# Kernel tuning notes

Hardware: AMD Instinct MI355X
Metric: run time of the kernel (lower is better)

Reference implementation:

```python
import jax, jax.numpy as jnp
import numpy as np

# torch.optim.Adam defaults
LR = 1e-3
B1 = 0.9
B2 = 0.999
EPS = 1e-8


def setup_inputs() -> dict:
    key = jax.random.key(0)
    k1, k2 = jax.random.split(key)
    B, N_train, d = 128, 16384, 1024
    h = jax.random.normal(k1, (B, d), dtype=jnp.float32)
    H_train = jax.random.normal(k2, (N_train, d), dtype=jnp.float32)
    return {"h": h, "H_train": H_train, "n_epoch": 1000}


def reference(h, H_train, n_epoch):
    # preweights: [B, N_train], optimized by Adam for n_epoch steps
    B, N_train = h.shape[0], H_train.shape[0]

    def loss_fn(p):
        w = jax.nn.softmax(p, axis=-1)          # [B, N_train]
        H_approx = w @ H_train                   # [B, d]
        return jnp.sum((H_approx - h) ** 2)

    grad_fn = jax.grad(loss_fn)

    def step(carry, t):
        p, m, v = carry
        g = grad_fn(p)
        m = B1 * m + (1.0 - B1) * g
        v = B2 * v + (1.0 - B2) * (g * g)
        m_hat = m / (1.0 - B1 ** t)
        v_hat = v / (1.0 - B2 ** t)
        p = p - LR * m_hat / (jnp.sqrt(v_hat) + EPS)
        return (p, m, v), None

    z = jnp.zeros((B, N_train), dtype=jnp.float32)
    ts = jnp.arange(1, n_epoch + 1, dtype=jnp.float32)
    (p, _, _), _ = jax.lax.scan(step, (z, z, z), ts)
    return jax.nn.softmax(p, axis=-1)
```

## Files before the change

kernel.cpp:

```cpp
#include <hip/hip_runtime.h>
#include <math.h>

#define BB 128
#define NTR 16384
#define DD 1024
#define PN (BB*NTR)
#define CN (BB*DD)
#define HN (NTR*DD)
#define FWD_SLABS 64
#define BWD_SLABS 4

typedef short bf16x8 __attribute__((ext_vector_type(8)));
typedef float f32x2  __attribute__((ext_vector_type(2)));
typedef float f32x4v __attribute__((ext_vector_type(4)));

__device__ __forceinline__ ushort f2bf(float f) {
  uint u = __float_as_uint(f);
  return (ushort)((u + 0x7FFFu + ((u >> 16) & 1u)) >> 16);
}
__device__ __forceinline__ float bf2f(ushort h) { return __uint_as_float(((uint)h) << 16); }
__device__ __forceinline__ void split2(float f, ushort& a, ushort& b) {
  a = f2bf(f); float r1 = f - bf2f(a);
  b = f2bf(r1);
}

__global__ __launch_bounds__(256) void k_prep(const float* __restrict__ H,
    ushort* __restrict__ H0, ushort* __restrict__ H1)
{
  const size_t i = ((size_t)blockIdx.x * 256 + threadIdx.x) * 4;
  const float4 x = *(const float4*)(H + i);
  ushort a[4], b[4];
  split2(x.x, a[0], b[0]); split2(x.y, a[1], b[1]);
  split2(x.z, a[2], b[2]); split2(x.w, a[3], b[3]);
  *(ushort4*)(H0 + i) = make_ushort4(a[0], a[1], a[2], a[3]);
  *(ushort4*)(H1 + i) = make_ushort4(b[0], b[1], b[2], b[3]);
}

__global__ __launch_bounds__(256) void k_stat0(float* __restrict__ pmx, float* __restrict__ psm) {
  const int i = blockIdx.x * 256 + threadIdx.x;
  pmx[i] = 0.f;
  psm[i] = 2048.f;
}
__global__ __launch_bounds__(256) void k_einit(float* __restrict__ e) {
  const size_t base = (size_t)blockIdx.x * 2048 + threadIdx.x * 8;
  const float4 one = make_float4(1.f, 1.f, 1.f, 1.f);
  *(float4*)(e + base) = one;
  *(float4*)(e + base + 4) = one;
}

__device__ __forceinline__ void combine_stats(const float* __restrict__ pmx,
    const float* __restrict__ psm, int row, float& mx, float& inv)
{
  mx = -INFINITY;
#pragma unroll
  for (int c = 0; c < 8; ++c) mx = fmaxf(mx, pmx[c*128 + row]);
  float s = 0.f;
#pragma unroll
  for (int c = 0; c < 8; ++c) s += psm[c*128 + row] * expf(pmx[c*128 + row] - mx);
  inv = 1.0f / s;
}

__global__ __launch_bounds__(512) void k_softmax_f(const float* __restrict__ p,
                                                   float* __restrict__ w) {
  const int row = blockIdx.x, tid = threadIdx.x;
  const float* pr = p + (size_t)row * NTR;
  float x[32]; float mx = -INFINITY;
#pragma unroll
  for (int i = 0; i < 32; ++i) { x[i] = pr[i*512 + tid]; mx = fmaxf(mx, x[i]); }
  __shared__ float red[512];
  red[tid] = mx; __syncthreads();
  for (int s = 256; s > 0; s >>= 1) { if (tid < s) red[tid] = fmaxf(red[tid], red[tid+s]); __syncthreads(); }
  mx = red[0]; __syncthreads();
  float sum = 0.f;
#pragma unroll
  for (int i = 0; i < 32; ++i) { x[i] = expf(x[i] - mx); sum += x[i]; }
  red[tid] = sum; __syncthreads();
  for (int s = 256; s > 0; s >>= 1) { if (tid < s) red[tid] += red[tid+s]; __syncthreads(); }
  const float inv = 1.0f / red[0];
  float* wr = w + (size_t)row * NTR;
#pragma unroll
  for (int i = 0; i < 32; ++i) wr[i*512 + tid] = x[i] * inv;
}

__global__ __launch_bounds__(256) void k_fwd_v(const float* __restrict__ e,
    const float* __restrict__ pmx, const float* __restrict__ psm,
    const float* __restrict__ H, float* __restrict__ Cp)
{
  const int nt = blockIdx.x, tid = threadIdx.x;
  const int kbase = blockIdx.y * 256;
  const int chunk = kbase >> 11;
  Cp += (size_t)blockIdx.y * CN;
  __shared__ float As[2][8][128];
  __shared__ float Bs[2][8][128];
  __shared__ float sscale[128];
  if (tid < 128) {
    float mx, inv; combine_stats(pmx, psm, tid, mx, inv);
    sscale[tid] = expf(pmx[chunk*128 + tid] - mx) * inv;
  }
  const int tm = tid >> 4, tn = tid & 15;
  const int m0 = tm * 8, n0 = tn * 8;
  const int mm = tid >> 1, q = tid & 1;
  const int br = tid >> 5, bc = (tid & 31) * 4;
  const float* Asrc = e + (size_t)mm*NTR + kbase + q*4;
  const float* Bsrc = H + (size_t)(kbase+br)*DD + nt*128 + bc;
  __syncthreads();
  const float sA = sscale[mm];

  f32x2 acc[8][4];
#pragma unroll
  for (int i = 0; i < 8; ++i)
#pragma unroll
    for (int j = 0; j < 4; ++j) acc[i][j] = (f32x2){0.f, 0.f};

  float4 ra = *(const float4*)(Asrc);
  float4 rb = *(const float4*)(Bsrc);
  As[0][q*4+0][mm]=ra.x*sA; As[0][q*4+1][mm]=ra.y*sA;
  As[0][q*4+2][mm]=ra.z*sA; As[0][q*4+3][mm]=ra.w*sA;
  *(float4*)&Bs[0][br][bc] = rb;
  ra = *(const float4*)(Asrc + 8);
  rb = *(const float4*)(Bsrc + (size_t)8*DD);

  for (int t = 0; t < 32; ++t) {
    const int cur = t & 1;
    __syncthreads();
    if (t + 1 < 32) {
      As[cur^1][q*4+0][mm]=ra.x*sA; As[cur^1][q*4+1][mm]=ra.y*sA;
      As[cur^1][q*4+2][mm]=ra.z*sA; As[cur^1][q*4+3][mm]=ra.w*sA;
      *(float4*)&Bs[cur^1][br][bc] = rb;
    }
    if (t + 2 < 32) {
      ra = *(const float4*)(Asrc + (t+2)*8);
      rb = *(const float4*)(Bsrc + (size_t)((t+2)*8)*DD);
    }
#pragma unroll
    for (int k = 0; k < 8; ++k) {
      float a[8];
      *(float4*)&a[0] = *(const float4*)&As[cur][k][m0];
      *(float4*)&a[4] = *(const float4*)&As[cur][k][m0+4];
      const float4 b01 = *(const float4*)&Bs[cur][k][n0];
      const float4 b23 = *(const float4*)&Bs[cur][k][n0+4];
      f32x2 b[4];
      b[0] = (f32x2){b01.x, b01.y}; b[1] = (f32x2){b01.z, b01.w};
      b[2] = (f32x2){b23.x, b23.y}; b[3] = (f32x2){b23.z, b23.w};
#pragma unroll
      for (int i = 0; i < 8; ++i) {
        const f32x2 ai = (f32x2){a[i], a[i]};
#pragma unroll
        for (int j = 0; j < 4; ++j)
          acc[i][j] = __builtin_elementwise_fma(ai, b[j], acc[i][j]);
      }
    }
  }
#pragma unroll
  for (int i = 0; i < 8; ++i) {
    float* dst = Cp + (size_t)(m0+i)*DD + nt*128 + n0;
    *(float4*)dst     = make_float4(acc[i][0].x, acc[i][0].y, acc[i][1].x, acc[i][1].y);
    *(float4*)(dst+4) = make_float4(acc[i][2].x, acc[i][2].y, acc[i][3].x, acc[i][3].y);
  }
}

__global__ __launch_bounds__(256) void k_reduce_S2s(const float* __restrict__ X,
    const float* __restrict__ h,
    ushort* __restrict__ s0, ushort* __restrict__ s1)
{
  const size_t off = ((size_t)blockIdx.x * 256 + threadIdx.x) * 2;
  f32x2 s = (f32x2){0.f, 0.f};
#pragma unroll 4
  for (int k = 0; k < FWD_SLABS; ++k) {
    const f32x2 c = *(const f32x2*)(X + (size_t)k * CN + off);
    s.x += c.x; s.y += c.y;
  }
  const f32x2 hh = *(const f32x2*)(h + off);
  float v0 = 2.f*(s.x-hh.x), v1 = 2.f*(s.y-hh.y);
  ushort a0, b0, a1, b1;
  split2(v0, a0, b0); split2(v1, a1, b1);
  *(ushort2*)(s0 + off) = make_ushort2(a0, a1);
  *(ushort2*)(s1 + off) = make_ushort2(b0, b1);
}

__global__ __launch_bounds__(256, 4) void k_gemm3_bwd(
    const ushort* __restrict__ A0, const ushort* __restrict__ A1,
    const ushort* __restrict__ B0, const ushort* __restrict__ B1,
    const float* __restrict__ e,
    const float* __restrict__ pmx, const float* __restrict__ psm,
    float* __restrict__ C, float* __restrict__ rpart)
{
  __shared__ ushort lds[12288];
  __shared__ float rbuf[128][2];
  __shared__ float sscale[128];
  const int tid = threadIdx.x;
  const int lane = tid & 63, wid = tid >> 6;
  const int wm = (wid >> 1) * 64, wn = (wid & 1) * 32;
  const int bn = blockIdx.x, ks = blockIdx.y;
  const int n0 = bn * 64;
  const int chunk = n0 >> 11;
  const int kbase = ks * 256;
  C += (size_t)ks * PN;

  if (tid < 128) {
    float mx, inv; combine_stats(pmx, psm, tid, mx, inv);
    sscale[tid] = expf(pmx[chunk*128 + tid] - mx) * inv;
  }

  const ushort* Ap[2] = {A0, A1};
  const ushort* Bp[2] = {B0, B1};

  f32x4v acc[4][2];
#pragma unroll
  for (int i = 0; i < 4; ++i)
#pragma unroll
    for (int j = 0; j < 2; ++j) acc[i][j] = (f32x4v){0.f, 0.f, 0.f, 0.f};

  for (int kt = 0; kt < 8; ++kt) {
    const int kpos = kbase + (kt << 5);
#pragma unroll
    for (int c = 0; c < 4; ++c) {
      const int L = c*256 + tid;
      const int s = L >> 9, rr = L & 511;
      const int row = rr >> 2, slot = rr & 3;
      const int sl = slot ^ ((row >> 1) & 3);
      const ushort* src = Ap[s] + (size_t)row * DD + kpos + (sl << 3);
      __builtin_amdgcn_global_load_lds((const __attribute__((address_space(1))) void*)src,
          (__attribute__((address_space(3))) void*)&lds[(size_t)(c*256 + (wid << 6)) * 8], 16, 0, 0);
    }
#pragma unroll
    for (int c = 0; c < 2; ++c) {
      const int L = c*256 + tid;
      const int s = L >> 8, rr = L & 255;
      const int row = rr >> 2, slot = rr & 3;
      const int sl = slot ^ ((row >> 1) & 3);
      const ushort* src = Bp[s] + (size_t)(n0 + row) * DD + kpos + (sl << 3);
      __builtin_amdgcn_global_load_lds((const __attribute__((address_space(1))) void*)src,
          (__attribute__((address_space(3))) void*)&lds[8192 + (size_t)(c*256 + (wid << 6)) * 8], 16, 0, 0);
    }
    __syncthreads();

    bf16x8 bf[2][2];
#pragma unroll
    for (int s = 0; s < 2; ++s)
#pragma unroll
      for (int j = 0; j < 2; ++j) {
        const int n = wn + j*16 + (lane & 15);
        const int sl = (lane >> 4) ^ ((n >> 1) & 3);
        bf[s][j] = *(const bf16x8*)&lds[8192 + s*2048 + n*32 + sl*8];
      }
#pragma unroll
    for (int sa = 0; sa < 2; ++sa) {
      bf16x8 af[4];
#pragma unroll
      for (int i = 0; i < 4; ++i) {
        const int mrow = wm + i*16 + (lane & 15);
        const int sl = (lane >> 4) ^ ((mrow >> 1) & 3);
        af[i] = *(const bf16x8*)&lds[sa*4096 + mrow*32 + sl*8];
      }
#pragma unroll
      for (int sb = 0; sb < 2 - sa; ++sb)
#pragma unroll
        for (int i = 0; i < 4; ++i)
#pragma unroll
          for (int j = 0; j < 2; ++j)
            acc[i][j] = __builtin_amdgcn_mfma_f32_16x16x32_bf16(af[i], bf[sb][j], acc[i][j], 0, 0, 0);
    }
    __syncthreads();
  }
#pragma unroll
  for (int i = 0; i < 4; ++i) {
    const int rbase = wm + i*16 + ((lane >> 4) << 2);
#pragma unroll
    for (int r = 0; r < 4; ++r) {
      const int row = rbase + r;
      const float sc = sscale[row];
      float s = 0.f;
#pragma unroll
      for (int j = 0; j < 2; ++j) {
        const int cg = n0 + wn + j*16 + (lane & 15);
        C[(size_t)row * NTR + cg] = acc[i][j][r];
        s = fmaf(e[(size_t)row * NTR + cg] * sc, acc[i][j][r], s);
      }
      s += __shfl_xor(s, 1); s += __shfl_xor(s, 2);
      s += __shfl_xor(s, 4); s += __shfl_xor(s, 8);
      if ((lane & 15) == 0) rbuf[row][wid & 1] = s;
    }
  }
  __syncthreads();
  if (tid < 128)
    rpart[(size_t)tid * 1024 + ks*256 + bn] = rbuf[tid][0] + rbuf[tid][1];
}

__global__ __launch_bounds__(256) void k_adam_f(float* __restrict__ pp_,
    float* __restrict__ m, float* __restrict__ v,
    float* __restrict__ e, const float* __restrict__ X,
    const float* __restrict__ rpart,
    const float* __restrict__ pmx_in, const float* __restrict__ psm_in,
    float* __restrict__ pmx_out, float* __restrict__ psm_out,
    float bc1, float bc2)
{
  const int bid = blockIdx.x, tid = threadIdx.x;
  const int row = bid >> 3, chunk = bid & 7;
  float mx, inv; combine_stats(pmx_in, psm_in, row, mx, inv);
  const float sc = expf(pmx_in[chunk*128 + row] - mx) * inv;
  __shared__ float red[256];
  {
    const float* rr_ = rpart + (size_t)row * 1024;
    red[tid] = rr_[tid] + rr_[tid + 256] + rr_[tid + 512] + rr_[tid + 768];
  }
  __syncthreads();
  for (int s = 128; s > 0; s >>= 1) { if (tid < s) red[tid] += red[tid+s]; __syncthreads(); }
  const float rr = red[0];
  const size_t base = (size_t)bid * 2048 + tid * 4;
  float pn[8];
#pragma unroll
  for (int part = 0; part < 2; ++part) {
    const size_t off = base + part * 1024;
    float4 u  = *(const float4*)(X + off);
    const float4 u1 = *(const float4*)(X + (size_t)PN + off);
    const float4 u2 = *(const float4*)(X + (size_t)2*PN + off);
    const float4 u3 = *(const float4*)(X + (size_t)3*PN + off);
    u.x += u1.x + u2.x + u3.x; u.y += u1.y + u2.y + u3.y;
    u.z += u1.z + u2.z + u3.z; u.w += u1.w + u2.w + u3.w;
    const float4 e4 = *(const float4*)(e + off);
    const float wv[4] = {e4.x*sc, e4.y*sc, e4.z*sc, e4.w*sc};
    const float uu[4] = {u.x, u.y, u.z, u.w};
    float4 p4 = *(float4*)(pp_ + off);
    float4 m4 = *(float4*)(m + off);
    float4 v4 = *(float4*)(v + off);
    float* pp = (float*)&p4; float* mm = (float*)&m4; float* vv = (float*)&v4;
#pragma unroll
    for (int e2 = 0; e2 < 4; ++e2) {
      const float g  = wv[e2] * (uu[e2] - rr);
      const float mn = 0.9f*mm[e2] + 0.1f*g;
      const float vn = 0.999f*vv[e2] + 0.001f*(g*g);
      const float mh = mn / bc1, vh = vn / bc2;
      pp[e2] = pp[e2] - 1e-3f * mh / (sqrtf(vh) + 1e-8f);
      mm[e2] = mn; vv[e2] = vn;
      pn[part*4 + e2] = pp[e2];
    }
    *(float4*)(pp_ + off) = p4;
    *(float4*)(m + off) = m4;
    *(float4*)(v + off) = v4;
  }
  float lmx = pn[0];
#pragma unroll
  for (int e2 = 1; e2 < 8; ++e2) lmx = fmaxf(lmx, pn[e2]);
  __syncthreads();
  red[tid] = lmx; __syncthreads();
  for (int s = 128; s > 0; s >>= 1) { if (tid < s) red[tid] = fmaxf(red[tid], red[tid+s]); __syncthreads(); }
  const float bmx = red[0]; __syncthreads();
  float en[8];
  float ls = 0.f;
#pragma unroll
  for (int e2 = 0; e2 < 8; ++e2) { en[e2] = expf(pn[e2] - bmx); ls += en[e2]; }
#pragma unroll
  for (int part = 0; part < 2; ++part) {
    const size_t off = base + part * 1024;
    *(float4*)(e + off) = make_float4(en[part*4+0], en[part*4+1], en[part*4+2], en[part*4+3]);
  }
  red[tid] = ls; __syncthreads();
  for (int s = 128; s > 0; s >>= 1) { if (tid < s) red[tid] += red[tid+s]; __syncthreads(); }
  if (tid == 0) {
    pmx_out[chunk*128 + row] = bmx;
    psm_out[chunk*128 + row] = red[0];
  }
}

extern "C" void kernel_launch(void* const* d_in, const int* in_sizes, int n_in,
                              void* d_out, int out_size, void* d_ws, size_t ws_size,
                              hipStream_t stream) {
  const float* h = (const float*)d_in[0];
  const float* H = (const float*)d_in[1];
  (void)in_sizes; (void)n_in; (void)out_size; (void)ws_size;
  const int n_epoch = 1000;

  float* p  = (float*)d_ws;
  float* m  = p + PN;
  float* v  = m + PN;
  float* e  = v + PN;
  float* X  = e + PN;
  float* rp = X + (size_t)4*PN;
  float* pmxA = rp + 128*1024;
  float* psmA = pmxA + 1024;
  float* pmxB = psmA + 1024;
  float* psmB = pmxB + 1024;
  ushort* s0 = (ushort*)(psmB + 1024);
  ushort* s1 = s0 + CN;
  ushort* H0 = s1 + CN, *H1 = H0 + HN;

  hipMemsetAsync(p, 0, (size_t)3*PN*sizeof(float), stream);
  k_prep<<<HN/1024, 256, 0, stream>>>(H, H0, H1);
  k_stat0<<<4, 256, 0, stream>>>(pmxA, psmA);
  k_einit<<<PN/2048, 256, 0, stream>>>(e);

  for (int s = 1; s <= n_epoch; ++s) {
    float* pmx_in  = (s & 1) ? pmxA : pmxB;
    float* psm_in  = (s & 1) ? psmA : psmB;
    float* pmx_out = (s & 1) ? pmxB : pmxA;
    float* psm_out = (s & 1) ? psmB : psmA;
    k_fwd_v<<<dim3(8, FWD_SLABS), 256, 0, stream>>>(e, pmx_in, psm_in, H, X);
    k_reduce_S2s<<<CN/512, 256, 0, stream>>>(X, h, s0, s1);
    k_gemm3_bwd<<<dim3(256, BWD_SLABS), 256, 0, stream>>>(s0, s1, H0, H1, e, pmx_in, psm_in, X, rp);
    const float bc1 = 1.0f - powf(0.9f,   (float)s);
    const float bc2 = 1.0f - powf(0.999f, (float)s);
    k_adam_f<<<1024, 256, 0, stream>>>(p, m, v, e, X, rp, pmx_in, psm_in, pmx_out, psm_out, bc1, bc2);
  }
  k_softmax_f<<<BB, 512, 0, stream>>>(p, (float*)d_out);
}
```

Measured before the change: 114.1 ms.

## Replace split-K backward GEMM with full-K narrower N tiles

The backward GEMM used to split K=1024 into 4 slabs, writing 4 partial [B,N] outputs that the Adam kernel then summed. It now runs full K in each block with a 32-column N tile over 512 blocks. The goal is to drop three extra PN-sized writes and reads per epoch and shrink the rpart reduction. In exchange, each block loops 4x longer over K, A-tile reuse per block is lower, and the grid has half as many blocks.

Result: no change. 115.8 ms (+1.5%).

```diff
diff --git a/kernel.cpp b/kernel.cpp
--- a/kernel.cpp
+++ b/kernel.cpp
@@ -8,7 +8,6 @@
 #define CN (BB*DD)
 #define HN (NTR*DD)
 #define FWD_SLABS 64
-#define BWD_SLABS 4
 
 typedef short bf16x8 __attribute__((ext_vector_type(8)));
 typedef float f32x2  __attribute__((ext_vector_type(2)));
@@ -178,24 +177,22 @@
   *(ushort2*)(s1 + off) = make_ushort2(b0, b1);
 }
 
-__global__ __launch_bounds__(256, 4) void k_gemm3_bwd(
+__global__ __launch_bounds__(256, 2) void k_gemm3_bwd(
     const ushort* __restrict__ A0, const ushort* __restrict__ A1,
     const ushort* __restrict__ B0, const ushort* __restrict__ B1,
     const float* __restrict__ e,
     const float* __restrict__ pmx, const float* __restrict__ psm,
     float* __restrict__ C, float* __restrict__ rpart)
 {
-  __shared__ ushort lds[12288];
+  __shared__ ushort lds[10240];
   __shared__ float rbuf[128][2];
   __shared__ float sscale[128];
   const int tid = threadIdx.x;
   const int lane = tid & 63, wid = tid >> 6;
-  const int wm = (wid >> 1) * 64, wn = (wid & 1) * 32;
-  const int bn = blockIdx.x, ks = blockIdx.y;
-  const int n0 = bn * 64;
+  const int wm = (wid >> 1) * 64, wn = (wid & 1) * 16;
+  const int bn = blockIdx.x;
+  const int n0 = bn * 32;
   const int chunk = n0 >> 11;
-  const int kbase = ks * 256;
-  C += (size_t)ks * PN;
 
   if (tid < 128) {
     float mx, inv; combine_stats(pmx, psm, tid, mx, inv);
@@ -205,14 +202,12 @@
   const ushort* Ap[2] = {A0, A1};
   const ushort* Bp[2] = {B0, B1};
 
-  f32x4v acc[4][2];
-#pragma unroll
-  for (int i = 0; i < 4; ++i)
-#pragma unroll
-    for (int j = 0; j < 2; ++j) acc[i][j] = (f32x4v){0.f, 0.f, 0.f, 0.f};
-
-  for (int kt = 0; kt < 8; ++kt) {
-    const int kpos = kbase + (kt << 5);
+  f32x4v acc[4];
+#pragma unroll
+  for (int i = 0; i < 4; ++i) acc[i] = (f32x4v){0.f, 0.f, 0.f, 0.f};
+
+  for (int kt = 0; kt < 32; ++kt) {
+    const int kpos = kt << 5;
 #pragma unroll
     for (int c = 0; c < 4; ++c) {
       const int L = c*256 + tid;
@@ -223,27 +218,23 @@
       __builtin_amdgcn_global_load_lds((const __attribute__((address_space(1))) void*)src,
           (__attribute__((address_space(3))) void*)&lds[(size_t)(c*256 + (wid << 6)) * 8], 16, 0, 0);
     }
-#pragma unroll
-    for (int c = 0; c < 2; ++c) {
-      const int L = c*256 + tid;
-      const int s = L >> 8, rr = L & 255;
+    {
+      const int s = tid >> 7, rr = tid & 127;
       const int row = rr >> 2, slot = rr & 3;
       const int sl = slot ^ ((row >> 1) & 3);
       const ushort* src = Bp[s] + (size_t)(n0 + row) * DD + kpos + (sl << 3);
       __builtin_amdgcn_global_load_lds((const __attribute__((address_space(1))) void*)src,
-          (__attribute__((address_space(3))) void*)&lds[8192 + (size_t)(c*256 + (wid << 6)) * 8], 16, 0, 0);
+          (__attribute__((address_space(3))) void*)&lds[8192 + (size_t)(wid << 6) * 8], 16, 0, 0);
     }
     __syncthreads();
 
-    bf16x8 bf[2][2];
-#pragma unroll
-    for (int s = 0; s < 2; ++s)
-#pragma unroll
-      for (int j = 0; j < 2; ++j) {
-        const int n = wn + j*16 + (lane & 15);
-        const int sl = (lane >> 4) ^ ((n >> 1) & 3);
-        bf[s][j] = *(const bf16x8*)&lds[8192 + s*2048 + n*32 + sl*8];
-      }
+    bf16x8 bf[2];
+#pragma unroll
+    for (int s = 0; s < 2; ++s) {
+      const int n = wn + (lane & 15);
+      const int sl = (lane >> 4) ^ ((n >> 1) & 3);
+      bf[s] = *(const bf16x8*)&lds[8192 + s*1024 + n*32 + sl*8];
+    }
 #pragma unroll
     for (int sa = 0; sa < 2; ++sa) {
       bf16x8 af[4];
@@ -257,9 +248,7 @@
       for (int sb = 0; sb < 2 - sa; ++sb)
 #pragma unroll
         for (int i = 0; i < 4; ++i)
-#pragma unroll
-          for (int j = 0; j < 2; ++j)
-            acc[i][j] = __builtin_amdgcn_mfma_f32_16x16x32_bf16(af[i], bf[sb][j], acc[i][j], 0, 0, 0);
+          acc[i] = __builtin_amdgcn_mfma_f32_16x16x32_bf16(af[i], bf[sb], acc[i], 0, 0, 0);
     }
     __syncthreads();
   }
@@ -269,14 +258,9 @@
 #pragma unroll
     for (int r = 0; r < 4; ++r) {
       const int row = rbase + r;
-      const float sc = sscale[row];
-      float s = 0.f;
-#pragma unroll
-      for (int j = 0; j < 2; ++j) {
-        const int cg = n0 + wn + j*16 + (lane & 15);
-        C[(size_t)row * NTR + cg] = acc[i][j][r];
-        s = fmaf(e[(size_t)row * NTR + cg] * sc, acc[i][j][r], s);
-      }
+      const int cg = n0 + wn + (lane & 15);
+      C[(size_t)row * NTR + cg] = acc[i][r];
+      float s = e[(size_t)row * NTR + cg] * sscale[row] * acc[i][r];
       s += __shfl_xor(s, 1); s += __shfl_xor(s, 2);
       s += __shfl_xor(s, 4); s += __shfl_xor(s, 8);
       if ((lane & 15) == 0) rbuf[row][wid & 1] = s;
@@ -284,7 +268,7 @@
   }
   __syncthreads();
   if (tid < 128)
-    rpart[(size_t)tid * 1024 + ks*256 + bn] = rbuf[tid][0] + rbuf[tid][1];
+    rpart[(size_t)tid * 512 + bn] = rbuf[tid][0] + rbuf[tid][1];
 }
 
 __global__ __launch_bounds__(256) void k_adam_f(float* __restrict__ pp_,
@@ -300,10 +284,7 @@
   float mx, inv; combine_stats(pmx_in, psm_in, row, mx, inv);
   const float sc = expf(pmx_in[chunk*128 + row] - mx) * inv;
   __shared__ float red[256];
-  {
-    const float* rr_ = rpart + (size_t)row * 1024;
-    red[tid] = rr_[tid] + rr_[tid + 256] + rr_[tid + 512] + rr_[tid + 768];
-  }
+  red[tid] = rpart[(size_t)row*512 + tid] + rpart[(size_t)row*512 + 256 + tid];
   __syncthreads();
   for (int s = 128; s > 0; s >>= 1) { if (tid < s) red[tid] += red[tid+s]; __syncthreads(); }
   const float rr = red[0];
@@ -312,12 +293,7 @@
 #pragma unroll
   for (int part = 0; part < 2; ++part) {
     const size_t off = base + part * 1024;
-    float4 u  = *(const float4*)(X + off);
-    const float4 u1 = *(const float4*)(X + (size_t)PN + off);
-    const float4 u2 = *(const float4*)(X + (size_t)2*PN + off);
-    const float4 u3 = *(const float4*)(X + (size_t)3*PN + off);
-    u.x += u1.x + u2.x + u3.x; u.y += u1.y + u2.y + u3.y;
-    u.z += u1.z + u2.z + u3.z; u.w += u1.w + u2.w + u3.w;
+    const float4 u = *(const float4*)(X + off);
     const float4 e4 = *(const float4*)(e + off);
     const float wv[4] = {e4.x*sc, e4.y*sc, e4.z*sc, e4.w*sc};
     const float uu[4] = {u.x, u.y, u.z, u.w};
@@ -377,7 +353,7 @@
   float* e  = v + PN;
   float* X  = e + PN;
   float* rp = X + (size_t)4*PN;
-  float* pmxA = rp + 128*1024;
+  float* pmxA = rp + 128*512;
   float* psmA = pmxA + 1024;
   float* pmxB = psmA + 1024;
   float* psmB = pmxB + 1024;
@@ -397,7 +373,7 @@
     float* psm_out = (s & 1) ? psmB : psmA;
     k_fwd_v<<<dim3(8, FWD_SLABS), 256, 0, stream>>>(e, pmx_in, psm_in, H, X);
     k_reduce_S2s<<<CN/512, 256, 0, stream>>>(X, h, s0, s1);
-    k_gemm3_bwd<<<dim3(256, BWD_SLABS), 256, 0, stream>>>(s0, s1, H0, H1, e, pmx_in, psm_in, X, rp);
+    k_gemm3_bwd<<<512, 256, 0, stream>>>(s0, s1, H0, H1, e, pmx_in, psm_in, X, rp);
     const float bc1 = 1.0f - powf(0.9f,   (float)s);
     const float bc2 = 1.0f - powf(0.999f, (float)s);
     k_adam_f<<<1024, 256, 0, stream>>>(p, m, v, e, X, rp, pmx_in, psm_in, pmx_out, psm_out, bc1, bc2);
```
